# Kernel optimization log

Measured on AMD Instinct MI355X. Metric: run time of the kernel, lower is better.

Reference implementation:

```python
import jax, jax.numpy as jnp
import numpy as np

T, B, I, H, R, O = 128, 32, 128, 128, 100, 64


def setup_inputs() -> dict:
    key = jax.random.key(0)
    ks = jax.random.split(key, 8)
    # xavier-ish / kaiming-ish scales so tanh doesn't saturate
    return {
        "x": jax.random.normal(ks[0], (T, B, I), jnp.float32),
        "C": jax.random.uniform(ks[1], (R, R), jnp.float32) / R,
        "W_ih": jax.random.normal(ks[2], (R, I, H), jnp.float32) * (1.0 / np.sqrt(I)),
        "W_hh": jax.random.normal(ks[3], (R, H, H), jnp.float32) * (1.0 / np.sqrt(H)),
        "W_rhh": jax.random.normal(ks[4], (R, H, H), jnp.float32) * (1.0 / np.sqrt(H)),
        "bias": jax.random.normal(ks[5], (R, H), jnp.float32) * 0.1,
        "W_out": jax.random.normal(ks[6], (R * H, O), jnp.float32) * (1.0 / np.sqrt(R * H)),
        "b_out": jax.random.normal(ks[7], (O,), jnp.float32) * 0.1,
    }


def reference(x, C, W_ih, W_hh, W_rhh, bias, b_out, W_out):
    seq_len, bs, _ = x.shape
    num_regions, hidden = bias.shape
    H0 = jnp.zeros((num_regions, bs, hidden), dtype=x.dtype)

    def step(Hprev, x_t):
        # input drive: per-region projection of the shared input
        inp = jnp.einsum('bi,rih->rbh', x_t, W_ih)
        # local recurrence
        loc = jnp.einsum('rbh,rhg->rbg', Hprev, W_hh)
        # connectome-weighted message sum: recurrent_sum[j] = sum_i C[i,j] * Hprev[i]
        msg = jnp.einsum('ij,ibh->jbh', C, Hprev)
        cross = jnp.einsum('rbh,rhg->rbg', msg, W_rhh)
        Ht = jnp.tanh(inp + loc + cross + bias[:, None, :])
        return Ht, Ht

    _, H_hist = jax.lax.scan(step, H0, x)          # [T, R, B, H]
    H_hist = H_hist.transpose(0, 2, 1, 3).reshape(seq_len, bs, num_regions * hidden)
    return H_hist @ W_out + b_out                   # [T, B, O]
```

## Files before the change

kernel.cpp:

```cpp
#include <hip/hip_runtime.h>
#include <hip/hip_bf16.h>

typedef unsigned char u8;
typedef unsigned short u16;
typedef __attribute__((ext_vector_type(8))) short bf16x8;
typedef __attribute__((ext_vector_type(8))) _Float16 f16x8;
typedef __attribute__((ext_vector_type(4))) float f32x4;
typedef __attribute__((ext_vector_type(2))) float f32x2;
typedef __attribute__((ext_vector_type(4))) int i32x4;

#define T_ 128
#define B_ 32
#define I_ 128
#define H_ 128
#define R_ 100
#define O_ 64
#define NWG2 200
#define NRED 4
#define SLICE (R_*B_*H_)
#define ROWB  (B_*H_)
#define XOFF  (T_*B_*I_)
#define WOFF  (R_*H_*H_)
#define OOFF  (O_*R_*H_)
#define PB    (16*O_)
#define SFBASE 6400
#define XCNTOFF 7168

__device__ __forceinline__ float b2f(u16 u) {
  unsigned x = ((unsigned)u) << 16; float f; __builtin_memcpy(&f, &x, 4); return f;
}
__device__ __forceinline__ u16 f2b(float f) {
  unsigned x; __builtin_memcpy(&x, &f, 4);
  unsigned lsb = (x >> 16) & 1u;
  x += 0x7fffu + lsb;
  return (u16)(x >> 16);
}
__device__ __forceinline__ void split2(float f, u16& hi, u16& lo) {
  hi = f2b(f);
  lo = f2b(f - b2f(hi));
}
__device__ __forceinline__ u16 f2h(float f) {
  _Float16 h = (_Float16)f; u16 u; __builtin_memcpy(&u, &h, 2); return u;
}
__device__ __forceinline__ float h2f(u16 u) {
  _Float16 h; __builtin_memcpy(&h, &u, 2); return (float)h;
}
__device__ __forceinline__ void split2h(float f, u16& hi, u16& lo) {
  _Float16 h = (_Float16)f;
  _Float16 l = (_Float16)(f - (float)h);
  __builtin_memcpy(&hi, &h, 2); __builtin_memcpy(&lo, &l, 2);
}
__device__ __forceinline__ float fast_tanh(float v) {
  float a = fabsf(v);
  float e = __expf(-2.f * a);
  float th = (1.f - e) * __builtin_amdgcn_rcpf(1.f + e);
  return v < 0.f ? -th : th;
}

#if __has_builtin(__builtin_amdgcn_cvt_pk_f32_fp8) && __has_builtin(__builtin_amdgcn_cvt_pk_fp8_f32)
#define HW_FP8 1
#endif

__device__ __forceinline__ unsigned enc1_fp8(float f) {
  unsigned x; __builtin_memcpy(&x, &f, 4);
  unsigned s = (x >> 31) << 7;
  float a = fabsf(f);
  if (!(a < 464.f)) return s | 0x7E;
  if (a == 0.f) return s;
  int E = (int)((x >> 23) & 0xFF) - 127;
  if (E < -6) E = -6;
  float sc; unsigned sb = (unsigned)(127 + 3 - E) << 23; __builtin_memcpy(&sc, &sb, 4);
  int q = (int)rintf(a * sc);
  if (q == 16) { E += 1; q = 8; }
  if (E > 8) return s | 0x7E;
  unsigned ee, mm;
  if (q < 8) { ee = 0; mm = (unsigned)q; }
  else { ee = (unsigned)(E + 7); mm = (unsigned)(q - 8); }
  return s | (ee << 3) | mm;
}
__device__ __forceinline__ float dec1_fp8(unsigned b) {
  unsigned s = (b >> 7) & 1, ee = (b >> 3) & 0xF, mm = b & 7;
  float v;
  if (ee == 0) v = (float)mm * 0.001953125f;
  else { unsigned fb = ((ee + 120) << 23) | (mm << 20); __builtin_memcpy(&v, &fb, 4); }
  return s ? -v : v;
}
__device__ __forceinline__ void fp8x4_to_f32(unsigned u, float* o) {
#ifdef HW_FP8
  f32x2 a = __builtin_amdgcn_cvt_pk_f32_fp8((int)u, false);
  f32x2 b = __builtin_amdgcn_cvt_pk_f32_fp8((int)u, true);
  o[0] = a[0]; o[1] = a[1]; o[2] = b[0]; o[3] = b[1];
#else
  o[0] = dec1_fp8(u & 255); o[1] = dec1_fp8((u >> 8) & 255);
  o[2] = dec1_fp8((u >> 16) & 255); o[3] = dec1_fp8(u >> 24);
#endif
}
__device__ __forceinline__ unsigned f32x4_to_fp8(float f0, float f1, float f2, float f3) {
#ifdef HW_FP8
  int v = __builtin_amdgcn_cvt_pk_fp8_f32(f0, f1, 0, false);
  v = __builtin_amdgcn_cvt_pk_fp8_f32(f2, f3, v, true);
  return (unsigned)v;
#else
  return enc1_fp8(f0) | (enc1_fp8(f1) << 8) | (enc1_fp8(f2) << 16) | (enc1_fp8(f3) << 24);
#endif
}
__device__ __forceinline__ i32x4 pack16(const u16* p) {
  i32x4 o;
  #pragma unroll
  for (int g = 0; g < 4; ++g)
    o[g] = (int)f32x4_to_fp8(h2f(p[g*4+0]), h2f(p[g*4+1]), h2f(p[g*4+2]), h2f(p[g*4+3]));
  return o;
}

__device__ __forceinline__ void st16_sc(void* p, i32x4 v) {
  asm volatile("global_store_dwordx4 %0, %1, off sc1" :: "v"(p), "v"(v) : "memory");
}
__device__ __forceinline__ void ld4_issue0(int& r, const void* p) {
  asm volatile("global_load_dword %0, %1, off sc0" : "=v"(r) : "v"(p));
}
__device__ __forceinline__ void wait_vm() { asm volatile("s_waitcnt vmcnt(0)" ::: "memory"); }
#define WAITV(N) do { asm volatile("s_waitcnt vmcnt(" #N ")" ::: "memory"); \
                      __builtin_amdgcn_sched_barrier(0); } while (0)

__device__ __forceinline__ float aldf(const float* p) {
  return __hip_atomic_load((float*)p, __ATOMIC_RELAXED, __HIP_MEMORY_SCOPE_AGENT);
}
__device__ __forceinline__ void astf(float* p, float v) {
  __hip_atomic_store(p, v, __ATOMIC_RELAXED, __HIP_MEMORY_SCOPE_AGENT);
}

__global__ void __launch_bounds__(256)
probe_dtype(const u16* __restrict__ x, int* __restrict__ mode)
{
  __shared__ int cnt;
  if (threadIdx.x == 0) cnt = 0;
  __syncthreads();
  int bad = 0;
  for (int i = threadIdx.x; i < 8192; i += 256) {
    int ex = (x[i] >> 7) & 0xFF;
    if (ex >= 134) ++bad;
  }
  atomicAdd(&cnt, bad);
  __syncthreads();
  if (threadIdx.x == 0) *mode = (cnt > 256) ? 1 : 0;
}

__device__ __forceinline__ float load_in(const void* p, size_t i, int f32) {
  return f32 ? ((const float*)p)[i] : b2f(((const u16*)p)[i]);
}

__global__ void __launch_bounds__(256)
conv_split(const void* __restrict__ src, u16* __restrict__ hi, u16* __restrict__ lo,
           const int* __restrict__ mode, int n)
{
  int i = blockIdx.x * 256 + threadIdx.x;
  if (i < n) { u16 h, l; split2(load_in(src, i, *mode), h, l); hi[i] = h; lo[i] = l; }
}

__global__ void __launch_bounds__(256)
conv_vec(const void* __restrict__ src, float* __restrict__ dst,
         const int* __restrict__ mode, int n)
{
  int i = blockIdx.x * 256 + threadIdx.x;
  if (i < n) dst[i] = load_in(src, i, *mode);
}

__global__ void __launch_bounds__(256)
transpose_kn2(const void* __restrict__ in, u16* __restrict__ ohi, u16* __restrict__ olo,
              int KK, int NN, const int* __restrict__ mode, int fmt)
{
  __shared__ float tile[32][33];
  const int f32 = *mode;
  int ntk = KK >> 5, ntn = NN >> 5;
  int bid = blockIdx.x;
  int m  = bid / (ntk * ntn);
  int rem = bid % (ntk * ntn);
  int kt = rem / ntn, nt = rem % ntn;
  size_t base = (size_t)m * KK * NN;
  int tid = threadIdx.x;
  int tc = tid & 31, tr0 = tid >> 5;
  #pragma unroll
  for (int rr = 0; rr < 4; ++rr) {
    int tr = tr0 + rr * 8;
    tile[tr][tc] = load_in(in, base + (size_t)(kt*32 + tr) * NN + nt*32 + tc, f32);
  }
  __syncthreads();
  #pragma unroll
  for (int rr = 0; rr < 4; ++rr) {
    int tr = tr0 + rr * 8;
    u16 h, l;
    if (fmt) split2h(tile[tc][tr], h, l); else split2(tile[tc][tr], h, l);
    size_t di = base + (size_t)(nt*32 + tr) * KK + kt*32 + tc;
    ohi[di] = h; olo[di] = l;
  }
}

__device__ __forceinline__ void wait_flags(const int* f, int cnt, int target, int tid) {
  if (tid < cnt) {
    int sp = 0;
    while (__hip_atomic_load((int*)&f[tid * 32], __ATOMIC_RELAXED, __HIP_MEMORY_SCOPE_AGENT) < target) {
      __builtin_amdgcn_s_sleep(2);
      if (++sp > (1 << 18)) break;
    }
  }
  asm volatile("" ::: "memory");
  __syncthreads();
}
__device__ __forceinline__ void poll1(const int* f, int target) {
  int sp = 0;
  while (__hip_atomic_load((int*)f, __ATOMIC_RELAXED, __HIP_MEMORY_SCOPE_AGENT) < target) {
    if (++sp > 48) __builtin_amdgcn_s_sleep(2);
    if (sp > (1 << 20)) break;
  }
  asm volatile("" ::: "memory");
}
__device__ __forceinline__ void post_flag(int* f, int v) {
  __hip_atomic_store(f, v, __ATOMIC_RELAXED, __HIP_MEMORY_SCOPE_AGENT);
}

__device__ __forceinline__ f32x4 mfma_(bf16x8 a, bf16x8 b, f32x4 c) {
  return __builtin_amdgcn_mfma_f32_16x16x32_bf16(a, b, c, 0, 0, 0);
}
__device__ __forceinline__ f32x4 mfma_h(f16x8 a, f16x8 b, f32x4 c) {
  return __builtin_amdgcn_mfma_f32_16x16x32_f16(a, b, c, 0, 0, 0);
}

#define MIXROW(Q, CI) do { \
  float c_ = csh[(CI)]; float tf_[4]; \
  fp8x4_to_f32((unsigned)(Q), tf_); \
  macc0 = fmaf(c_, tf_[0], macc0); macc1 = fmaf(c_, tf_[1], macc1); \
  macc2 = fmaf(c_, tf_[2], macc2); macc3 = fmaf(c_, tf_[3], macc3); \
} while (0)

#define ISSUE8(Q, P) do { _Pragma("unroll") \
  for (int k_ = 0; k_ < 8; ++k_) ld4_issue0(Q[k_], (P) + (size_t)k_ * ROWB); } while (0)
#define ISSUE4(Q, P) do { _Pragma("unroll") \
  for (int k_ = 0; k_ < 4; ++k_) ld4_issue0(Q[k_], (P) + (size_t)k_ * ROWB); } while (0)
#define PROC8(Q, CI) do { _Pragma("unroll") \
  for (int k_ = 0; k_ < 8; ++k_) MIXROW(Q[k_], (CI) + k_); } while (0)
#define PROC4(Q, CI) do { _Pragma("unroll") \
  for (int k_ = 0; k_ < 4; ++k_) MIXROW(Q[k_], (CI) + k_); } while (0)

__global__ void __launch_bounds__(512, 2)
rnn_kernel(const u16* __restrict__ x,
           u8* __restrict__ Hb,
           const u16* __restrict__ WihT, const u16* __restrict__ WhhT,
           const u16* __restrict__ WrhhT,
           const float* __restrict__ Cf,
           const float* __restrict__ biasf,
           const u16* __restrict__ WoutT,
           float* __restrict__ part,
           u16* __restrict__ part2,
           const float* __restrict__ boutf,
           float* __restrict__ out, int* __restrict__ flags, int bigpart)
{
  const int w    = blockIdx.x;
  const int tid  = threadIdx.x;
  const int lane = tid & 63;
  const int wv   = tid >> 6;
  const int l15  = lane & 15;
  const int quad = lane >> 4;

  __shared__ __align__(16) u16 Hmhi[16 * 136];
  __shared__ __align__(16) u16 Hmlo[16 * 136];
  __shared__ __align__(16) u16 msgS[16 * 136];
  __shared__ __align__(16) u16 mS[16 * 128];
  __shared__ float csh[112];
  __shared__ int shRank;

  if (w >= NWG2) {
    const int aw = w - NWG2;
    for (int t = 0; t < T_; ++t) {
      wait_flags(flags + 1, NWG2, t + 1, tid);
      const float* pb = part + (size_t)(t & 1) * (NWG2 * PB);
      int e = aw * 512 + tid;
      int b = e >> 6, o = e & 63;
      int ue = b >> 4, bl = b & 15;
      float s = 0.f;
      #pragma unroll 4
      for (int r2 = 0; r2 < R_; ++r2)
        s += aldf(pb + (size_t)(r2 * 2 + ue) * PB + bl * O_ + o);
      out[(size_t)t * (B_*O_) + e] = s + boutf[o];
    }
    return;
  }

  int xcd;
  asm volatile("s_getreg_b32 %0, hwreg(HW_REG_XCC_ID)" : "=s"(xcd));
  xcd &= 7;
  if (tid == 0)
    shRank = __hip_atomic_fetch_add(&flags[XCNTOFF + xcd], 1,
                                    __ATOMIC_RELAXED, __HIP_MEMORY_SCOPE_AGENT);

  const int r = w >> 1;
  const int u = w & 1;
  const int col = wv * 16 + l15;

  for (int e = tid; e < 16 * 136; e += 512) { Hmhi[e] = 0; Hmlo[e] = 0; }
  if (tid < R_) csh[tid] = Cf[(size_t)tid * R_ + r];
  __syncthreads();
  const int rank = shRank;

  bf16x8 w0h[4], w0l[4], w1h[4], w1l[4];
  f16x8  w2h[4], w2l[4];
  bf16x8 boh[4], bol[4];
  {
    const u16* B0 = WihT  + (size_t)r * (H_*I_) + (size_t)col * 128;
    const u16* B1 = WhhT  + (size_t)r * (H_*H_) + (size_t)col * 128;
    const u16* B2 = WrhhT + (size_t)r * (H_*H_) + (size_t)col * 128;
    const int o = (wv >= 4) ? ((wv - 4) * 16 + l15) : l15;
    const u16* Bo = WoutT + (size_t)o * (R_*H_) + (size_t)r * H_;
    #pragma unroll
    for (int kk = 0; kk < 4; ++kk) {
      int koff = kk * 32 + quad * 8;
      w0h[kk] = *(const bf16x8*)(B0 + koff);
      w0l[kk] = *(const bf16x8*)(B0 + WOFF + koff);
      w1h[kk] = *(const bf16x8*)(B1 + koff);
      w1l[kk] = *(const bf16x8*)(B1 + WOFF + koff);
      w2h[kk] = *(const f16x8*)(B2 + koff);
      w2l[kk] = *(const f16x8*)(B2 + WOFF + koff);
      boh[kk] = *(const bf16x8*)(Bo + koff);
      bol[kk] = *(const bf16x8*)(Bo + OOFF + koff);
    }
  }
  const float bs = biasf[r*H_ + col];

  for (int t = 0; t < T_; ++t) {
    f32x4 accX = {0,0,0,0}, accH = {0,0,0,0};
    {
      const u16* Ax = x + (size_t)t * (B_*I_) + (size_t)(u*16) * I_;
      #pragma unroll
      for (int kk = 0; kk < 4; ++kk) {
        int koff = kk * 32 + quad * 8;
        const u16* pa = Ax + (size_t)l15 * 128 + koff;
        bf16x8 ah = *(const bf16x8*)pa, al = *(const bf16x8*)(pa + XOFF);
        accX = mfma_(al, w0h[kk], mfma_(ah, w0l[kk], mfma_(ah, w0h[kk], accX)));
        bf16x8 hh = *(const bf16x8*)(&Hmhi[l15 * 136 + koff]);
        bf16x8 hl = *(const bf16x8*)(&Hmlo[l15 * 136 + koff]);
        accH = mfma_(hl, w1h[kk], mfma_(hh, w1l[kk], mfma_(hh, w1h[kk], accH)));
      }
    }

    if (t > 0) {
      const int par = (t + 1) & 1;
      int* invf = &flags[SFBASE + ((xcd << 1) + par) * 32];

      if (rank == 0) {
        if (tid < NWG2) poll1(&flags[tid * 32], t);
        __syncthreads();
        if (tid == 0) {
          __builtin_amdgcn_fence(__ATOMIC_ACQUIRE, "agent");
          wait_vm();
          post_flag(invf, t);
        }
        __syncthreads();
      } else {
        if (tid == 0) poll1(invf, t);
        __syncthreads();
      }

      const u8* Hs = Hb + (size_t)par * SLICE
                   + (size_t)(u*16 + (tid >> 5)) * H_ + (tid & 31) * 4;
      float macc0=0.f, macc1=0.f, macc2=0.f, macc3=0.f;
      int bufA[8], bufB[8], bufC[8];
      const u8* pI = Hs;
      ISSUE8(bufA, pI); pI += (size_t)8 * ROWB;
      ISSUE8(bufB, pI); pI += (size_t)8 * ROWB;
      ISSUE8(bufC, pI); pI += (size_t)8 * ROWB;
      int ci = 0;
      for (int it = 0; it < 3; ++it) {
        WAITV(16); PROC8(bufA, ci); ci += 8; ISSUE8(bufA, pI); pI += (size_t)8 * ROWB;
        WAITV(16); PROC8(bufB, ci); ci += 8; ISSUE8(bufB, pI); pI += (size_t)8 * ROWB;
        WAITV(16); PROC8(bufC, ci); ci += 8; ISSUE8(bufC, pI); pI += (size_t)8 * ROWB;
      }
      WAITV(16); PROC8(bufA, 72); ISSUE4(bufA, pI);
      WAITV(12); PROC8(bufB, 80);
      WAITV(4);  PROC8(bufC, 88);
      WAITV(0);  PROC4(bufA, 96);

      union { u16 h[4]; unsigned long long v; } mw;
      mw.h[0]=f2h(macc0); mw.h[1]=f2h(macc1); mw.h[2]=f2h(macc2); mw.h[3]=f2h(macc3);
      *(unsigned long long*)&msgS[(tid >> 5) * 136 + (tid & 31) * 4] = mw.v;
      __syncthreads();

      #pragma unroll
      for (int kk = 0; kk < 4; ++kk) {
        int koff = kk * 32 + quad * 8;
        f16x8 a0 = *(const f16x8*)(&msgS[l15 * 136 + koff]);
        accX = mfma_h(a0, w2l[kk], mfma_h(a0, w2h[kk], accX));
      }
    } else {
      __syncthreads();
    }

    {
      #pragma unroll
      for (int rr = 0; rr < 4; ++rr) {
        int br = quad*4 + rr;
        u16 h, l;
        float v = fast_tanh(accX[rr] + accH[rr] + bs);
        split2(v, h, l);
        Hmhi[br*136 + col] = h; Hmlo[br*136 + col] = l;
        mS[br*128 + col] = f2h(v);
      }
    }
    __syncthreads();

    if (tid < 64) {
      int row = tid >> 2, c = (tid & 3) * 32;
      u8* Hn = Hb + (size_t)(t & 1) * SLICE + (size_t)r * ROWB
             + (size_t)(u*16 + row) * H_ + c;
      const u16* p = &mS[row * 128 + c];
      st16_sc(Hn,      pack16(p));
      st16_sc(Hn + 16, pack16(p + 16));
      wait_vm();
      if (tid == 0) post_flag(&flags[w * 32 + 0], t + 1);
    }

    {
      if (wv >= 4) {
        const int o = (wv - 4) * 16 + l15;
        f32x4 y0 = {0,0,0,0};
        #pragma unroll
        for (int kk = 0; kk < 4; ++kk) {
          int koff = kk * 32 + quad * 8;
          bf16x8 ah = *(const bf16x8*)(&Hmhi[l15 * 136 + koff]);
          bf16x8 al = *(const bf16x8*)(&Hmlo[l15 * 136 + koff]);
          y0 = mfma_(al, boh[kk], mfma_(ah, bol[kk], mfma_(ah, boh[kk], y0)));
        }
        if (bigpart) {
          u16* pp = part2 + ((size_t)t * R_ + r) * (B_*O_);
          #pragma unroll
          for (int rr = 0; rr < 4; ++rr)
            pp[(u*16 + quad*4 + rr)*O_ + o] = f2b(y0[rr]);
        } else {
          float* pp = part + (size_t)(t & 1) * (NWG2 * PB) + (size_t)w * PB;
          #pragma unroll
          for (int rr = 0; rr < 4; ++rr)
            astf(pp + (quad*4 + rr)*O_ + o, y0[rr]);
        }
      }
      if (!bigpart) {
        __syncthreads();
        if (tid == 0) post_flag(&flags[w * 32 + 1], t + 1);
      }
    }
  }
}

__global__ void __launch_bounds__(256)
reduce_out(const u16* __restrict__ part2, const float* __restrict__ boutf,
           float* __restrict__ out)
{
  const int t = blockIdx.x, tid = threadIdx.x;
  const u16* base = part2 + (size_t)t * R_ * (B_*O_) + tid * 8;
  float acc[8] = {0,0,0,0,0,0,0,0};
  for (int r2 = 0; r2 < R_; ++r2) {
    bf16x8 v = *(const bf16x8*)(base + (size_t)r2 * (B_*O_));
    #pragma unroll
    for (int j = 0; j < 8; ++j) acc[j] += b2f((u16)v[j]);
  }
  int e = tid * 8;
  #pragma unroll
  for (int j = 0; j < 8; ++j)
    out[(size_t)t * (B_*O_) + e + j] = acc[j] + boutf[(e + j) & (O_-1)];
}

extern "C" void kernel_launch(void* const* d_in, const int* in_sizes, int n_in,
                              void* d_out, int out_size, void* d_ws, size_t ws_size,
                              hipStream_t stream) {
  const void* xp    = d_in[0];
  const void* Cp    = d_in[1];
  const void* Wih   = d_in[2];
  const void* Whh   = d_in[3];
  const void* Wrhh  = d_in[4];
  const void* biasp = d_in[5];
  const void* Wout  = d_in[6];
  const void* boutp = d_in[7];
  float* outp = (float*)d_out;

  char* ws = (char*)d_ws;
  size_t off = 0;
  auto carve = [&](size_t bytes) -> void* {
    void* p = ws + off;
    off += (bytes + 255) & ~(size_t)255;
    return p;
  };
  u16*   xb    = (u16*)carve((size_t)2 * XOFF * 2);
  u8*    Hb    = (u8*)carve((size_t)2 * SLICE);
  u16*   wihT  = (u16*)carve((size_t)2 * WOFF * 2);
  u16*   whhT  = (u16*)carve((size_t)2 * WOFF * 2);
  u16*   wrhhT = (u16*)carve((size_t)2 * WOFF * 2);
  u16*   woutT = (u16*)carve((size_t)2 * OOFF * 2);
  float* cfp   = (float*)carve((size_t)R_ * R_ * 4);
  float* biasf = (float*)carve((size_t)R_ * H_ * 4);
  float* boutf = (float*)carve((size_t)O_ * 4);
  float* partp = (float*)carve((size_t)2 * NWG2 * PB * 4);
  int*   flagp = (int*)carve((size_t)256 * 32 * 4);
  int*   modep = (int*)carve(256);
  size_t part2_bytes = (size_t)T_ * R_ * B_ * O_ * 2;
  u16*   part2 = (u16*)(ws + off);
  int bigpart = (off + part2_bytes) <= ws_size;

  hipMemsetAsync(flagp, 0, (size_t)256 * 32 * 4, stream);

  probe_dtype<<<dim3(1), dim3(256), 0, stream>>>((const u16*)xp, modep);
  conv_split<<<dim3((XOFF + 255)/256), dim3(256), 0, stream>>>(xp, xb, xb + XOFF, modep, XOFF);
  conv_vec<<<dim3((R_*H_ + 255)/256), dim3(256), 0, stream>>>(biasp, biasf, modep, R_*H_);
  conv_vec<<<dim3(1), dim3(256), 0, stream>>>(boutp, boutf, modep, O_);
  conv_vec<<<dim3((R_*R_ + 255)/256), dim3(256), 0, stream>>>(Cp, cfp, modep, R_*R_);

  transpose_kn2<<<dim3(R_ * 16), dim3(256), 0, stream>>>(Wih,  wihT,  wihT  + WOFF, I_, H_, modep, 0);
  transpose_kn2<<<dim3(R_ * 16), dim3(256), 0, stream>>>(Whh,  whhT,  whhT  + WOFF, H_, H_, modep, 0);
  transpose_kn2<<<dim3(R_ * 16), dim3(256), 0, stream>>>(Wrhh, wrhhT, wrhhT + WOFF, H_, H_, modep, 1);
  transpose_kn2<<<dim3(800),     dim3(256), 0, stream>>>(Wout, woutT, woutT + OOFF, R_ * H_, O_, modep, 0);

  int nblk = bigpart ? NWG2 : (NWG2 + NRED);
  rnn_kernel<<<dim3(nblk), dim3(512), 0, stream>>>(
      xb, Hb, wihT, whhT, wrhhT, cfp, biasf, woutT,
      partp, part2, boutf, outp, flagp, bigpart);

  if (bigpart)
    reduce_out<<<dim3(T_), dim3(256), 0, stream>>>(part2, boutf, outp);
}
```

Measured before the change: 1.010 ms.

## Replace per-XCD hierarchical barrier with direct flag polling and packed FMA mixing

Removes the two-level barrier, in which one leader workgroup per XCD polled all 200 producer flags and republished an XCD-local flag. Instead, every workgroup now polls the 100 flags of the workgroups sharing its batch half (u), then issues an acquire fence. This drops the extra hop through the leader, at the cost of more concurrent flag polling traffic. Separately, the connectome message accumulation now uses v_pk_fma_f32 on paired fp8-decoded values, with C stored duplicated in LDS, halving the FMA instruction count.

```diff
diff --git a/kernel.cpp b/kernel.cpp
--- a/kernel.cpp
+++ b/kernel.cpp
@@ -23,8 +23,6 @@
 #define WOFF  (R_*H_*H_)
 #define OOFF  (O_*R_*H_)
 #define PB    (16*O_)
-#define SFBASE 6400
-#define XCNTOFF 7168
 
 __device__ __forceinline__ float b2f(u16 u) {
   unsigned x = ((unsigned)u) << 16; float f; __builtin_memcpy(&f, &x, 4); return f;
@@ -85,15 +83,18 @@
   else { unsigned fb = ((ee + 120) << 23) | (mm << 20); __builtin_memcpy(&v, &fb, 4); }
   return s ? -v : v;
 }
+__device__ __forceinline__ void fp8x4_to_2x2(unsigned u, f32x2& a, f32x2& b) {
+#ifdef HW_FP8
+  a = __builtin_amdgcn_cvt_pk_f32_fp8((int)u, false);
+  b = __builtin_amdgcn_cvt_pk_f32_fp8((int)u, true);
+#else
+  a[0] = dec1_fp8(u & 255); a[1] = dec1_fp8((u >> 8) & 255);
+  b[0] = dec1_fp8((u >> 16) & 255); b[1] = dec1_fp8(u >> 24);
+#endif
+}
 __device__ __forceinline__ void fp8x4_to_f32(unsigned u, float* o) {
-#ifdef HW_FP8
-  f32x2 a = __builtin_amdgcn_cvt_pk_f32_fp8((int)u, false);
-  f32x2 b = __builtin_amdgcn_cvt_pk_f32_fp8((int)u, true);
+  f32x2 a, b; fp8x4_to_2x2(u, a, b);
   o[0] = a[0]; o[1] = a[1]; o[2] = b[0]; o[3] = b[1];
-#else
-  o[0] = dec1_fp8(u & 255); o[1] = dec1_fp8((u >> 8) & 255);
-  o[2] = dec1_fp8((u >> 16) & 255); o[3] = dec1_fp8(u >> 24);
-#endif
 }
 __device__ __forceinline__ unsigned f32x4_to_fp8(float f0, float f1, float f2, float f3) {
 #ifdef HW_FP8
@@ -110,6 +111,12 @@
   for (int g = 0; g < 4; ++g)
     o[g] = (int)f32x4_to_fp8(h2f(p[g*4+0]), h2f(p[g*4+1]), h2f(p[g*4+2]), h2f(p[g*4+3]));
   return o;
+}
+
+__device__ __forceinline__ f32x2 pk_fma(f32x2 a, f32x2 b, f32x2 c) {
+  f32x2 d;
+  asm("v_pk_fma_f32 %0, %1, %2, %3" : "=v"(d) : "v"(a), "v"(b), "v"(c));
+  return d;
 }
 
 __device__ __forceinline__ void st16_sc(void* p, i32x4 v) {
@@ -226,10 +233,10 @@
 }
 
 #define MIXROW(Q, CI) do { \
-  float c_ = csh[(CI)]; float tf_[4]; \
-  fp8x4_to_f32((unsigned)(Q), tf_); \
-  macc0 = fmaf(c_, tf_[0], macc0); macc1 = fmaf(c_, tf_[1], macc1); \
-  macc2 = fmaf(c_, tf_[2], macc2); macc3 = fmaf(c_, tf_[3], macc3); \
+  f32x2 c2_ = csh2[(CI)]; \
+  f32x2 a_, b_; fp8x4_to_2x2((unsigned)(Q), a_, b_); \
+  macc01 = pk_fma(a_, c2_, macc01); \
+  macc23 = pk_fma(b_, c2_, macc23); \
 } while (0)
 
 #define ISSUE8(Q, P) do { _Pragma("unroll") \
@@ -265,8 +272,7 @@
   __shared__ __align__(16) u16 Hmlo[16 * 136];
   __shared__ __align__(16) u16 msgS[16 * 136];
   __shared__ __align__(16) u16 mS[16 * 128];
-  __shared__ float csh[112];
-  __shared__ int shRank;
+  __shared__ __align__(16) f32x2 csh2[112];
 
   if (w >= NWG2) {
     const int aw = w - NWG2;
@@ -285,21 +291,17 @@
     return;
   }
 
-  int xcd;
-  asm volatile("s_getreg_b32 %0, hwreg(HW_REG_XCC_ID)" : "=s"(xcd));
-  xcd &= 7;
-  if (tid == 0)
-    shRank = __hip_atomic_fetch_add(&flags[XCNTOFF + xcd], 1,
-                                    __ATOMIC_RELAXED, __HIP_MEMORY_SCOPE_AGENT);
-
   const int r = w >> 1;
   const int u = w & 1;
   const int col = wv * 16 + l15;
 
   for (int e = tid; e < 16 * 136; e += 512) { Hmhi[e] = 0; Hmlo[e] = 0; }
-  if (tid < R_) csh[tid] = Cf[(size_t)tid * R_ + r];
+  if (tid < R_) {
+    float c = Cf[(size_t)tid * R_ + r];
+    f32x2 c2; c2[0] = c; c2[1] = c;
+    csh2[tid] = c2;
+  }
   __syncthreads();
-  const int rank = shRank;
 
   bf16x8 w0h[4], w0l[4], w1h[4], w1l[4];
   f16x8  w2h[4], w2l[4];
@@ -343,25 +345,15 @@
 
     if (t > 0) {
       const int par = (t + 1) & 1;
-      int* invf = &flags[SFBASE + ((xcd << 1) + par) * 32];
-
-      if (rank == 0) {
-        if (tid < NWG2) poll1(&flags[tid * 32], t);
-        __syncthreads();
-        if (tid == 0) {
-          __builtin_amdgcn_fence(__ATOMIC_ACQUIRE, "agent");
-          wait_vm();
-          post_flag(invf, t);
-        }
-        __syncthreads();
-      } else {
-        if (tid == 0) poll1(invf, t);
-        __syncthreads();
-      }
+
+      if (tid < R_) poll1(&flags[((tid << 1) | u) * 32], t);
+      __syncthreads();
+      if (tid == 0) __builtin_amdgcn_fence(__ATOMIC_ACQUIRE, "agent");
+      __syncthreads();
 
       const u8* Hs = Hb + (size_t)par * SLICE
                    + (size_t)(u*16 + (tid >> 5)) * H_ + (tid & 31) * 4;
-      float macc0=0.f, macc1=0.f, macc2=0.f, macc3=0.f;
+      f32x2 macc01 = {0.f, 0.f}, macc23 = {0.f, 0.f};
       int bufA[8], bufB[8], bufC[8];
       const u8* pI = Hs;
       ISSUE8(bufA, pI); pI += (size_t)8 * ROWB;
@@ -379,7 +371,8 @@
       WAITV(0);  PROC4(bufA, 96);
 
       union { u16 h[4]; unsigned long long v; } mw;
-      mw.h[0]=f2h(macc0); mw.h[1]=f2h(macc1); mw.h[2]=f2h(macc2); mw.h[3]=f2h(macc3);
+      mw.h[0]=f2h(macc01[0]); mw.h[1]=f2h(macc01[1]);
+      mw.h[2]=f2h(macc23[0]); mw.h[3]=f2h(macc23[1]);
       *(unsigned long long*)&msgS[(tid >> 5) * 136 + (tid & 31) * 4] = mw.v;
       __syncthreads();
 
```

New measurement: 1.111 ms. +10.0%, slower.

## Split connectome message reduction across two thread halves with dwordx2 loads and packed FMA

Applied to the files above, without the earlier changes.

Restructures the per-step message gather so each thread loads 8 fp8 values per row with dwordx2 loads and covers every other region row. The two 256-thread halves each take 50 of the 100 regions and combine their partial sums through shared memory. Accumulation uses v_pk_fma_f32 with a duplicated C coefficient. This cuts the load instruction count and FMA issue slots in the latency-critical recurrent step, at the cost of an extra barrier and an LDS reduction.

```diff
diff --git a/kernel.cpp b/kernel.cpp
--- a/kernel.cpp
+++ b/kernel.cpp
@@ -8,6 +8,7 @@
 typedef __attribute__((ext_vector_type(4))) float f32x4;
 typedef __attribute__((ext_vector_type(2))) float f32x2;
 typedef __attribute__((ext_vector_type(4))) int i32x4;
+typedef __attribute__((ext_vector_type(2))) int i32x2;
 
 #define T_ 128
 #define B_ 32
@@ -85,15 +86,18 @@
   else { unsigned fb = ((ee + 120) << 23) | (mm << 20); __builtin_memcpy(&v, &fb, 4); }
   return s ? -v : v;
 }
+__device__ __forceinline__ void fp8x4_to_2x2(unsigned u, f32x2& a, f32x2& b) {
+#ifdef HW_FP8
+  a = __builtin_amdgcn_cvt_pk_f32_fp8((int)u, false);
+  b = __builtin_amdgcn_cvt_pk_f32_fp8((int)u, true);
+#else
+  a[0] = dec1_fp8(u & 255); a[1] = dec1_fp8((u >> 8) & 255);
+  b[0] = dec1_fp8((u >> 16) & 255); b[1] = dec1_fp8(u >> 24);
+#endif
+}
 __device__ __forceinline__ void fp8x4_to_f32(unsigned u, float* o) {
-#ifdef HW_FP8
-  f32x2 a = __builtin_amdgcn_cvt_pk_f32_fp8((int)u, false);
-  f32x2 b = __builtin_amdgcn_cvt_pk_f32_fp8((int)u, true);
+  f32x2 a, b; fp8x4_to_2x2(u, a, b);
   o[0] = a[0]; o[1] = a[1]; o[2] = b[0]; o[3] = b[1];
-#else
-  o[0] = dec1_fp8(u & 255); o[1] = dec1_fp8((u >> 8) & 255);
-  o[2] = dec1_fp8((u >> 16) & 255); o[3] = dec1_fp8(u >> 24);
-#endif
 }
 __device__ __forceinline__ unsigned f32x4_to_fp8(float f0, float f1, float f2, float f3) {
 #ifdef HW_FP8
@@ -112,11 +116,17 @@
   return o;
 }
 
+__device__ __forceinline__ f32x2 pk_fma(f32x2 a, f32x2 b, f32x2 c) {
+  f32x2 d;
+  asm("v_pk_fma_f32 %0, %1, %2, %3" : "=v"(d) : "v"(a), "v"(b), "v"(c));
+  return d;
+}
+
 __device__ __forceinline__ void st16_sc(void* p, i32x4 v) {
   asm volatile("global_store_dwordx4 %0, %1, off sc1" :: "v"(p), "v"(v) : "memory");
 }
-__device__ __forceinline__ void ld4_issue0(int& r, const void* p) {
-  asm volatile("global_load_dword %0, %1, off sc0" : "=v"(r) : "v"(p));
+__device__ __forceinline__ void ld8_issue0(i32x2& r, const void* p) {
+  asm volatile("global_load_dwordx2 %0, %1, off sc0" : "=v"(r) : "v"(p));
 }
 __device__ __forceinline__ void wait_vm() { asm volatile("s_waitcnt vmcnt(0)" ::: "memory"); }
 #define WAITV(N) do { asm volatile("s_waitcnt vmcnt(" #N ")" ::: "memory"); \
@@ -225,21 +235,23 @@
   return __builtin_amdgcn_mfma_f32_16x16x32_f16(a, b, c, 0, 0, 0);
 }
 
-#define MIXROW(Q, CI) do { \
-  float c_ = csh[(CI)]; float tf_[4]; \
-  fp8x4_to_f32((unsigned)(Q), tf_); \
-  macc0 = fmaf(c_, tf_[0], macc0); macc1 = fmaf(c_, tf_[1], macc1); \
-  macc2 = fmaf(c_, tf_[2], macc2); macc3 = fmaf(c_, tf_[3], macc3); \
+#define MIXROW2(Q, CI) do { \
+  f32x2 c2_ = csh2[((CI) << 1) + half]; \
+  f32x2 a0_, a1_, b0_, b1_; \
+  fp8x4_to_2x2((unsigned)(Q)[0], a0_, a1_); \
+  fp8x4_to_2x2((unsigned)(Q)[1], b0_, b1_); \
+  macc0 = pk_fma(a0_, c2_, macc0); macc1 = pk_fma(a1_, c2_, macc1); \
+  macc2 = pk_fma(b0_, c2_, macc2); macc3 = pk_fma(b1_, c2_, macc3); \
 } while (0)
 
-#define ISSUE8(Q, P) do { _Pragma("unroll") \
-  for (int k_ = 0; k_ < 8; ++k_) ld4_issue0(Q[k_], (P) + (size_t)k_ * ROWB); } while (0)
-#define ISSUE4(Q, P) do { _Pragma("unroll") \
-  for (int k_ = 0; k_ < 4; ++k_) ld4_issue0(Q[k_], (P) + (size_t)k_ * ROWB); } while (0)
-#define PROC8(Q, CI) do { _Pragma("unroll") \
-  for (int k_ = 0; k_ < 8; ++k_) MIXROW(Q[k_], (CI) + k_); } while (0)
-#define PROC4(Q, CI) do { _Pragma("unroll") \
-  for (int k_ = 0; k_ < 4; ++k_) MIXROW(Q[k_], (CI) + k_); } while (0)
+#define ISSUE8P(Q, P) do { _Pragma("unroll") \
+  for (int k_ = 0; k_ < 8; ++k_) ld8_issue0(Q[k_], (P) + (size_t)k_ * (2*ROWB)); } while (0)
+#define ISSUE2P(Q, P) do { _Pragma("unroll") \
+  for (int k_ = 0; k_ < 2; ++k_) ld8_issue0(Q[k_], (P) + (size_t)k_ * (2*ROWB)); } while (0)
+#define PROC8P(Q, CI) do { _Pragma("unroll") \
+  for (int k_ = 0; k_ < 8; ++k_) MIXROW2(Q[k_], (CI) + k_); } while (0)
+#define PROC2P(Q, CI) do { _Pragma("unroll") \
+  for (int k_ = 0; k_ < 2; ++k_) MIXROW2(Q[k_], (CI) + k_); } while (0)
 
 __global__ void __launch_bounds__(512, 2)
 rnn_kernel(const u16* __restrict__ x,
@@ -265,7 +277,8 @@
   __shared__ __align__(16) u16 Hmlo[16 * 136];
   __shared__ __align__(16) u16 msgS[16 * 136];
   __shared__ __align__(16) u16 mS[16 * 128];
-  __shared__ float csh[112];
+  __shared__ __align__(16) f32x2 csh2[112];
+  __shared__ __align__(16) f32x2 redS[256][4];
   __shared__ int shRank;
 
   if (w >= NWG2) {
@@ -297,7 +310,11 @@
   const int col = wv * 16 + l15;
 
   for (int e = tid; e < 16 * 136; e += 512) { Hmhi[e] = 0; Hmlo[e] = 0; }
-  if (tid < R_) csh[tid] = Cf[(size_t)tid * R_ + r];
+  if (tid < R_) {
+    float c = Cf[(size_t)tid * R_ + r];
+    f32x2 c2; c2[0] = c; c2[1] = c;
+    csh2[tid] = c2;
+  }
   __syncthreads();
   const int rank = shRank;
 
@@ -359,28 +376,40 @@
         __syncthreads();
       }
 
-      const u8* Hs = Hb + (size_t)par * SLICE
-                   + (size_t)(u*16 + (tid >> 5)) * H_ + (tid & 31) * 4;
-      float macc0=0.f, macc1=0.f, macc2=0.f, macc3=0.f;
-      int bufA[8], bufB[8], bufC[8];
+      const int half = tid >> 8;
+      const int s    = tid & 255;
+      const int bb   = s >> 4;
+      const int h0   = (s & 15) * 8;
+      const u8* Hs = Hb + (size_t)par * SLICE + (size_t)half * ROWB
+                   + (size_t)(u*16 + bb) * H_ + h0;
+      f32x2 macc0 = {0.f,0.f}, macc1 = {0.f,0.f}, macc2 = {0.f,0.f}, macc3 = {0.f,0.f};
+      i32x2 bufA[8], bufB[8], bufC[8];
       const u8* pI = Hs;
-      ISSUE8(bufA, pI); pI += (size_t)8 * ROWB;
-      ISSUE8(bufB, pI); pI += (size_t)8 * ROWB;
-      ISSUE8(bufC, pI); pI += (size_t)8 * ROWB;
-      int ci = 0;
-      for (int it = 0; it < 3; ++it) {
-        WAITV(16); PROC8(bufA, ci); ci += 8; ISSUE8(bufA, pI); pI += (size_t)8 * ROWB;
-        WAITV(16); PROC8(bufB, ci); ci += 8; ISSUE8(bufB, pI); pI += (size_t)8 * ROWB;
-        WAITV(16); PROC8(bufC, ci); ci += 8; ISSUE8(bufC, pI); pI += (size_t)8 * ROWB;
-      }
-      WAITV(16); PROC8(bufA, 72); ISSUE4(bufA, pI);
-      WAITV(12); PROC8(bufB, 80);
-      WAITV(4);  PROC8(bufC, 88);
-      WAITV(0);  PROC4(bufA, 96);
-
-      union { u16 h[4]; unsigned long long v; } mw;
-      mw.h[0]=f2h(macc0); mw.h[1]=f2h(macc1); mw.h[2]=f2h(macc2); mw.h[3]=f2h(macc3);
-      *(unsigned long long*)&msgS[(tid >> 5) * 136 + (tid & 31) * 4] = mw.v;
+      ISSUE8P(bufA, pI); pI += (size_t)16 * ROWB;
+      ISSUE8P(bufB, pI); pI += (size_t)16 * ROWB;
+      ISSUE8P(bufC, pI); pI += (size_t)16 * ROWB;
+      WAITV(16); PROC8P(bufA, 0);  ISSUE8P(bufA, pI); pI += (size_t)16 * ROWB;
+      WAITV(16); PROC8P(bufB, 8);  ISSUE8P(bufB, pI); pI += (size_t)16 * ROWB;
+      WAITV(16); PROC8P(bufC, 16); ISSUE8P(bufC, pI); pI += (size_t)16 * ROWB;
+      WAITV(16); PROC8P(bufA, 24); ISSUE2P(bufA, pI);
+      WAITV(10); PROC8P(bufB, 32);
+      WAITV(2);  PROC8P(bufC, 40);
+      WAITV(0);  PROC2P(bufA, 48);
+
+      if (half) {
+        redS[s][0] = macc0; redS[s][1] = macc1;
+        redS[s][2] = macc2; redS[s][3] = macc3;
+      }
+      __syncthreads();
+      if (!half) {
+        f32x2 r0 = redS[s][0], r1 = redS[s][1], r2 = redS[s][2], r3 = redS[s][3];
+        union { u16 h[8]; i32x4 v; } mw;
+        mw.h[0] = f2h(macc0[0] + r0[0]); mw.h[1] = f2h(macc0[1] + r0[1]);
+        mw.h[2] = f2h(macc1[0] + r1[0]); mw.h[3] = f2h(macc1[1] + r1[1]);
+        mw.h[4] = f2h(macc2[0] + r2[0]); mw.h[5] = f2h(macc2[1] + r2[1]);
+        mw.h[6] = f2h(macc3[0] + r3[0]); mw.h[7] = f2h(macc3[1] + r3[1]);
+        *(i32x4*)&msgS[bb * 136 + h0] = mw.v;
+      }
       __syncthreads();
 
       #pragma unroll
```

Measured after the change: 1.071 ms. 6.0% more time.
